# Kernel optimization log

Hardware: AMD Instinct MI355X
Metric: run time of the kernel (lower is better)

The kernel has to match this reference:

```python
import jax, jax.numpy as jnp
import numpy as np

N_NODES = 50000
N_EDGES = 800000
HIDDEN = 128
N_LAYERS = 3
MAX_Z = 1000
N_GRAPHS = 512
LN_EPS = 1e-5


def setup_inputs() -> dict:
    key = jax.random.key(0)
    ks = jax.random.split(key, 16)
    s = 0.05
    inp = {
        "z": jax.random.randint(ks[0], (N_NODES,), 0, MAX_Z),
        "edge_index": jax.random.randint(ks[1], (2, N_EDGES), 0, N_NODES),
        "batch": jnp.sort(jax.random.randint(ks[2], (N_NODES,), 0, N_GRAPHS)),
        "z_table": jax.random.normal(ks[3], (MAX_Z, HIDDEN), jnp.float32) * s,
        "W1": jax.random.normal(ks[4], (N_LAYERS, HIDDEN, HIDDEN), jnp.float32) * s,
        "b1": jnp.zeros((N_LAYERS, HIDDEN), jnp.float32),
        "W2": jax.random.normal(ks[5], (N_LAYERS, HIDDEN, HIDDEN), jnp.float32) * s,
        "b2": jnp.zeros((N_LAYERS, HIDDEN), jnp.float32),
        "ln_g": jnp.ones((N_LAYERS, HIDDEN), jnp.float32),
        "ln_b": jnp.zeros((N_LAYERS, HIDDEN), jnp.float32),
        "lin1_W": jax.random.normal(ks[6], (N_LAYERS * HIDDEN, HIDDEN), jnp.float32) * s,
        "lin1_b": jnp.zeros((HIDDEN,), jnp.float32),
        "lin2_W": jax.random.normal(ks[7], (HIDDEN, 1), jnp.float32) * s,
        "lin2_b": jnp.zeros((1,), jnp.float32),
    }
    return inp


def _layernorm(h, g, b):
    mu = jnp.mean(h, axis=-1, keepdims=True)
    var = jnp.mean((h - mu) ** 2, axis=-1, keepdims=True)
    return g * (h - mu) * jax.lax.rsqrt(var + LN_EPS) + b


def _gin_conv(x, src, dst, W1, b1, W2, b2, g, b):
    # sum-aggregate neighbor features, eps = 0 (train_eps=False)
    agg = jax.ops.segment_sum(x[src], dst, num_segments=N_NODES)
    h = x + agg
    h = jax.nn.relu(h @ W1 + b1)
    h = jax.nn.relu(h @ W2 + b2)
    return _layernorm(h, g, b)


def reference(z, edge_index, batch, z_table, W1, b1, W2, b2, ln_g, ln_b,
              lin1_W, lin1_b, lin2_W, lin2_b):
    src, dst = edge_index[0], edge_index[1]
    x = z_table[z]  # [N, H] z embedding (z is 1-D so no sum over dim 1)
    xs = []
    for l in range(N_LAYERS):
        x = _gin_conv(x, src, dst, W1[l], b1[l], W2[l], b2[l], ln_g[l], ln_b[l])
        xs.append(x)
    xcat = jnp.concatenate(xs, axis=1)  # JK concat [N, L*H]
    # global mean pool over graphs
    sums = jax.ops.segment_sum(xcat, batch, num_segments=N_GRAPHS)
    cnts = jax.ops.segment_sum(jnp.ones((N_NODES, 1), xcat.dtype), batch,
                               num_segments=N_GRAPHS)
    pooled = sums / jnp.maximum(cnts, 1.0)
    h = jax.nn.relu(pooled @ lin1_W + lin1_b)
    # dropout is identity in eval mode
    return h @ lin2_W + lin2_b  # [N_GRAPHS, 1]
```

## Files before the change

kernel.cpp:

```cpp
#include <hip/hip_runtime.h>
#include <hip/hip_bf16.h>

#define NN 50000
#define NE 800000
#define HD 128
#define NL 3
#define NG 512
#define LN_EPS 1e-5f
#define NXCD 8
#define NPX 6250

typedef unsigned short u16;
typedef unsigned int u32;
typedef __attribute__((ext_vector_type(8))) short short8;
typedef __attribute__((ext_vector_type(4))) float f32x4;

__device__ __forceinline__ u16 f2bf(float f){
  u32 x = __float_as_uint(f);
  u32 r = (x + 0x7fffu + ((x >> 16) & 1u)) >> 16;
  return (u16)r;
}
__device__ __forceinline__ float blo(u32 u){ return __uint_as_float(u << 16); }
__device__ __forceinline__ float bhi(u32 u){ return __uint_as_float(u & 0xffff0000u); }
__device__ __forceinline__ u32 pk2(float a, float b){ return (u32)f2bf(a) | ((u32)f2bf(b) << 16); }

__device__ __forceinline__ int lower_bound_dev(const int* a, int n, int v){
  int lo = 0, hi = n;
  while (lo < hi){ int m = (lo + hi) >> 1; if (a[m] < v) lo = m + 1; else hi = m; }
  return lo;
}

__global__ __launch_bounds__(256) void k_prep_w(const float* __restrict__ W1,
    const float* __restrict__ W2, u16* __restrict__ Wt){
  int t = blockIdx.x * 256 + threadIdx.x;
  if (t >= 6 * 128 * 128) return;
  int w = t >> 14, r = t & 16383, n = r >> 7, k = r & 127;
  int l = w >> 1;
  const float* Ws = (w & 1) ? (W2 + l * 16384) : (W1 + l * 16384);
  Wt[t] = f2bf(Ws[k * 128 + n]);
}

__global__ __launch_bounds__(256) void k_embed(const int* __restrict__ z,
    const float* __restrict__ tab, u16* __restrict__ xb){
  int gt = blockIdx.x * 256 + threadIdx.x;
  int node = gt >> 5, q = gt & 31;
  float4 v = *reinterpret_cast<const float4*>(tab + (size_t)z[node] * 128 + q * 4);
  uint2 p = { pk2(v.x, v.y), pk2(v.z, v.w) };
  *reinterpret_cast<uint2*>(xb + (size_t)node * 128 + q * 4) = p;
}

__global__ __launch_bounds__(256) void k_count(const int* __restrict__ dst,
    int* __restrict__ deg){
  int xcd = blockIdx.x & 7;
  int grp = blockIdx.x >> 3;
  int nlo = xcd * NPX, nhi = nlo + NPX;
  for (int e = grp * 256 + threadIdx.x; e < NE; e += 128 * 256){
    int d = dst[e];
    if (d >= nlo && d < nhi) atomicAdd(&deg[d], 1);
  }
}

__global__ __launch_bounds__(256) void k_scan1(const int* __restrict__ deg,
    int* __restrict__ part, int* __restrict__ bsum){
  int i = blockIdx.x * 256 + threadIdx.x;
  int v = (i < NN) ? deg[i] : 0;
  int lane = threadIdx.x & 63, wave = threadIdx.x >> 6;
  int s = v;
  for (int off = 1; off < 64; off <<= 1){ int n = __shfl_up(s, off); if (lane >= off) s += n; }
  __shared__ int wsums[4];
  if (lane == 63) wsums[wave] = s;
  __syncthreads();
  int add = 0;
  for (int w = 0; w < wave; ++w) add += wsums[w];
  int incl = s + add;
  if (i < NN) part[i] = incl - v;
  if (threadIdx.x == 255) bsum[blockIdx.x] = incl;
}

__global__ __launch_bounds__(256) void k_scan2(int* __restrict__ bsum, int nb){
  int tid = threadIdx.x;
  int v = (tid < nb) ? bsum[tid] : 0;
  int lane = tid & 63, wave = tid >> 6;
  int s = v;
  for (int off = 1; off < 64; off <<= 1){ int n = __shfl_up(s, off); if (lane >= off) s += n; }
  __shared__ int wsums[4];
  if (lane == 63) wsums[wave] = s;
  __syncthreads();
  int add = 0;
  for (int w = 0; w < wave; ++w) add += wsums[w];
  int incl = s + add;
  if (tid < nb) bsum[tid] = incl - v;
}

__global__ __launch_bounds__(256) void k_scan3(const int* __restrict__ part,
    const int* __restrict__ bsum, int* __restrict__ rowptr, int* __restrict__ cursor){
  int i = blockIdx.x * 256 + threadIdx.x;
  if (i < NN){ int r = part[i] + bsum[blockIdx.x]; rowptr[i] = r; cursor[i] = r; }
  if (i == 0) rowptr[NN] = NE;
}

__global__ __launch_bounds__(256) void k_fill(const int* __restrict__ src,
    const int* __restrict__ dst, int* __restrict__ cursor, u16* __restrict__ col){
  int xcd = blockIdx.x & 7;
  int grp = blockIdx.x >> 3;
  int nlo = xcd * NPX, nhi = nlo + NPX;
  for (int e = grp * 256 + threadIdx.x; e < NE; e += 128 * 256){
    int d = dst[e];
    if (d >= nlo && d < nhi){
      int p = atomicAdd(&cursor[d], 1);
      col[p] = (u16)src[e];
    }
  }
}

__global__ __launch_bounds__(256) void k_gather(const int* __restrict__ rowptr,
    const u16* __restrict__ col, const u16* __restrict__ xb, u16* __restrict__ hb){
  int wave = threadIdx.x >> 6, lane = threadIdx.x & 63;
  int node = blockIdx.x * 4 + wave;
  int q = lane >> 4, l4 = lane & 15;
  float a[8] = {0.f,0.f,0.f,0.f,0.f,0.f,0.f,0.f};
  float b[8] = {0.f,0.f,0.f,0.f,0.f,0.f,0.f,0.f};
  if (q == 0){
    uint4 s = *reinterpret_cast<const uint4*>(xb + (size_t)node * 128 + l4 * 8);
    a[0] = blo(s.x); a[1] = bhi(s.x); a[2] = blo(s.y); a[3] = bhi(s.y);
    a[4] = blo(s.z); a[5] = bhi(s.z); a[6] = blo(s.w); a[7] = bhi(s.w);
  }
  int lo = rowptr[node], hi = rowptr[node + 1];
  int e = lo + q;
  for (; e + 4 < hi; e += 8){
    int c0 = col[e], c1 = col[e + 4];
    uint4 v0 = *reinterpret_cast<const uint4*>(xb + (size_t)c0 * 128 + l4 * 8);
    uint4 v1 = *reinterpret_cast<const uint4*>(xb + (size_t)c1 * 128 + l4 * 8);
    a[0] += blo(v0.x); a[1] += bhi(v0.x); a[2] += blo(v0.y); a[3] += bhi(v0.y);
    a[4] += blo(v0.z); a[5] += bhi(v0.z); a[6] += blo(v0.w); a[7] += bhi(v0.w);
    b[0] += blo(v1.x); b[1] += bhi(v1.x); b[2] += blo(v1.y); b[3] += bhi(v1.y);
    b[4] += blo(v1.z); b[5] += bhi(v1.z); b[6] += blo(v1.w); b[7] += bhi(v1.w);
  }
  if (e < hi){
    int c0 = col[e];
    uint4 v0 = *reinterpret_cast<const uint4*>(xb + (size_t)c0 * 128 + l4 * 8);
    a[0] += blo(v0.x); a[1] += bhi(v0.x); a[2] += blo(v0.y); a[3] += bhi(v0.y);
    a[4] += blo(v0.z); a[5] += bhi(v0.z); a[6] += blo(v0.w); a[7] += bhi(v0.w);
  }
  #pragma unroll
  for (int j = 0; j < 8; ++j){
    a[j] += b[j];
    a[j] += __shfl_xor(a[j], 16);
    a[j] += __shfl_xor(a[j], 32);
  }
  if (q == 0){
    uint4 p = { pk2(a[0], a[1]), pk2(a[2], a[3]), pk2(a[4], a[5]), pk2(a[6], a[7]) };
    *reinterpret_cast<uint4*>(hb + (size_t)node * 128 + l4 * 8) = p;
  }
}

__global__ __launch_bounds__(256) void k_layer(const u16* __restrict__ A,
    const u16* __restrict__ Wt1, const u16* __restrict__ Wt2,
    const float* __restrict__ bias1, const float* __restrict__ bias2,
    const float* __restrict__ lng, const float* __restrict__ lnb,
    u16* __restrict__ Cout){
  __shared__ u16 As[128 * 128];
  __shared__ u16 Ws[128 * 128];
  int tid = threadIdx.x;
  int rb = blockIdx.x * 128;

  #pragma unroll
  for (int i = 0; i < 8; ++i){
    int u = tid + i * 256;
    int n = u >> 4, k8 = u & 15;
    uint4 w = *reinterpret_cast<const uint4*>(Wt1 + n * 128 + k8 * 8);
    *reinterpret_cast<uint4*>(&Ws[n * 128 + (k8 ^ (n & 15)) * 8]) = w;
  }
  #pragma unroll
  for (int i = 0; i < 8; ++i){
    int u = tid + i * 256;
    int row = u >> 4, k8 = u & 15;
    int grow = rb + row;
    uint4 v = {0u, 0u, 0u, 0u};
    if (grow < NN) v = *reinterpret_cast<const uint4*>(A + (size_t)grow * 128 + k8 * 8);
    *reinterpret_cast<uint4*>(&As[row * 128 + (k8 ^ (row & 15)) * 8]) = v;
  }
  __syncthreads();

  uint4 w2r[8];
  #pragma unroll
  for (int i = 0; i < 8; ++i){
    int u = tid + i * 256;
    int n = u >> 4, k8 = u & 15;
    w2r[i] = *reinterpret_cast<const uint4*>(Wt2 + n * 128 + k8 * 8);
  }

  int wave = tid >> 6, lane = tid & 63;
  int lrow = lane & 15, kgrp = lane >> 4;
  f32x4 acc[2][8];
  #pragma unroll
  for (int rt = 0; rt < 2; ++rt)
    #pragma unroll
    for (int nt = 0; nt < 8; ++nt) acc[rt][nt] = (f32x4){0.f, 0.f, 0.f, 0.f};

  #pragma unroll
  for (int ks = 0; ks < 4; ++ks){
    int ch = ks * 4 + kgrp;
    short8 a0 = *reinterpret_cast<const short8*>(&As[(wave * 32 + lrow) * 128 + (ch ^ lrow) * 8]);
    short8 a1 = *reinterpret_cast<const short8*>(&As[(wave * 32 + 16 + lrow) * 128 + (ch ^ lrow) * 8]);
    #pragma unroll
    for (int nt = 0; nt < 8; ++nt){
      short8 b = *reinterpret_cast<const short8*>(&Ws[(nt * 16 + lrow) * 128 + (ch ^ lrow) * 8]);
      acc[0][nt] = __builtin_amdgcn_mfma_f32_16x16x32_bf16(a0, b, acc[0][nt], 0, 0, 0);
      acc[1][nt] = __builtin_amdgcn_mfma_f32_16x16x32_bf16(a1, b, acc[1][nt], 0, 0, 0);
    }
  }

  #pragma unroll
  for (int nt = 0; nt < 8; ++nt){
    float bv = __ldg(bias1 + nt * 16 + lrow);
    #pragma unroll
    for (int rt = 0; rt < 2; ++rt)
      #pragma unroll
      for (int j = 0; j < 4; ++j)
        acc[rt][nt][j] = fmaxf(acc[rt][nt][j] + bv, 0.f);
  }

  __syncthreads();

  #pragma unroll
  for (int i = 0; i < 8; ++i){
    int u = tid + i * 256;
    int n = u >> 4, k8 = u & 15;
    *reinterpret_cast<uint4*>(&Ws[n * 128 + (k8 ^ (n & 15)) * 8]) = w2r[i];
  }
  #pragma unroll
  for (int rt = 0; rt < 2; ++rt)
    #pragma unroll
    for (int j = 0; j < 4; ++j){
      int row = wave * 32 + rt * 16 + kgrp * 4 + j;
      #pragma unroll
      for (int nt = 0; nt < 8; ++nt){
        int col = nt * 16 + lrow;
        int ch = (col >> 3) ^ (row & 15);
        As[row * 128 + ch * 8 + (col & 7)] = f2bf(acc[rt][nt][j]);
      }
    }
  __syncthreads();

  #pragma unroll
  for (int rt = 0; rt < 2; ++rt)
    #pragma unroll
    for (int nt = 0; nt < 8; ++nt) acc[rt][nt] = (f32x4){0.f, 0.f, 0.f, 0.f};

  #pragma unroll
  for (int ks = 0; ks < 4; ++ks){
    int ch = ks * 4 + kgrp;
    short8 a0 = *reinterpret_cast<const short8*>(&As[(wave * 32 + lrow) * 128 + (ch ^ lrow) * 8]);
    short8 a1 = *reinterpret_cast<const short8*>(&As[(wave * 32 + 16 + lrow) * 128 + (ch ^ lrow) * 8]);
    #pragma unroll
    for (int nt = 0; nt < 8; ++nt){
      short8 b = *reinterpret_cast<const short8*>(&Ws[(nt * 16 + lrow) * 128 + (ch ^ lrow) * 8]);
      acc[0][nt] = __builtin_amdgcn_mfma_f32_16x16x32_bf16(a0, b, acc[0][nt], 0, 0, 0);
      acc[1][nt] = __builtin_amdgcn_mfma_f32_16x16x32_bf16(a1, b, acc[1][nt], 0, 0, 0);
    }
  }

  float gv[8], lbv[8];
  #pragma unroll
  for (int nt = 0; nt < 8; ++nt){
    int gcol = nt * 16 + lrow;
    float bv = __ldg(bias2 + gcol);
    gv[nt] = __ldg(lng + gcol); lbv[nt] = __ldg(lnb + gcol);
    #pragma unroll
    for (int rt = 0; rt < 2; ++rt)
      #pragma unroll
      for (int j = 0; j < 4; ++j)
        acc[rt][nt][j] = fmaxf(acc[rt][nt][j] + bv, 0.f);
  }
  #pragma unroll
  for (int rt = 0; rt < 2; ++rt)
    #pragma unroll
    for (int j = 0; j < 4; ++j){
      float s = 0.f, sq = 0.f;
      #pragma unroll
      for (int nt = 0; nt < 8; ++nt){ float v = acc[rt][nt][j]; s += v; sq += v * v; }
      #pragma unroll
      for (int off = 1; off < 16; off <<= 1){
        s += __shfl_xor(s, off); sq += __shfl_xor(sq, off);
      }
      float mu = s * (1.f / 128.f);
      float var = sq * (1.f / 128.f) - mu * mu;
      float rstd = rsqrtf(var + LN_EPS);
      #pragma unroll
      for (int nt = 0; nt < 8; ++nt)
        acc[rt][nt][j] = gv[nt] * (acc[rt][nt][j] - mu) * rstd + lbv[nt];
    }

  #pragma unroll
  for (int rt = 0; rt < 2; ++rt){
    int rbase = rb + wave * 32 + rt * 16 + kgrp * 4;
    #pragma unroll
    for (int nt = 0; nt < 8; ++nt){
      int gcol = nt * 16 + lrow;
      #pragma unroll
      for (int j = 0; j < 4; ++j){
        int grow = rbase + j;
        if (grow < NN) Cout[(size_t)grow * 128 + gcol] = f2bf(acc[rt][nt][j]);
      }
    }
  }
}

__global__ __launch_bounds__(256) void k_pool(const u16* __restrict__ xb,
    const int* __restrict__ batch, float* __restrict__ pooled, int lslice){
  int g = blockIdx.x;
  int w = threadIdx.x >> 6, lane = threadIdx.x & 63;
  __shared__ float red[4][128];
  int lo = lower_bound_dev(batch, NN, g);
  int hi = lower_bound_dev(batch, NN, g + 1);
  float s0 = 0.f, s1 = 0.f;
  for (int i = lo + w; i < hi; i += 4){
    u32 u = *reinterpret_cast<const u32*>(xb + (size_t)i * 128 + lane * 2);
    s0 += blo(u); s1 += bhi(u);
  }
  red[w][lane * 2] = s0; red[w][lane * 2 + 1] = s1;
  __syncthreads();
  int f = threadIdx.x;
  if (f < 128)
    pooled[(size_t)g * 384 + lslice * 128 + f] = red[0][f] + red[1][f] + red[2][f] + red[3][f];
}

__global__ __launch_bounds__(128) void k_final(const float* __restrict__ pooled,
    const int* __restrict__ batch, const float* __restrict__ W1,
    const float* __restrict__ b1, const float* __restrict__ W2,
    const float* __restrict__ b2, float* __restrict__ out){
  int g = blockIdx.x, f = threadIdx.x;
  int lo = lower_bound_dev(batch, NN, g);
  int hi = lower_bound_dev(batch, NN, g + 1);
  float scale = 1.f / fmaxf((float)(hi - lo), 1.f);
  __shared__ float p[384];
  for (int k = f; k < 384; k += 128) p[k] = pooled[(size_t)g * 384 + k] * scale;
  __syncthreads();
  float acc = __ldg(b1 + f);
  for (int k = 0; k < 384; ++k) acc += p[k] * __ldg(W1 + k * 128 + f);
  float hval = fmaxf(acc, 0.f);
  float v = hval * __ldg(W2 + f);
  for (int off = 32; off; off >>= 1) v += __shfl_xor(v, off);
  __shared__ float red[2];
  int lane = f & 63, wave = f >> 6;
  if (lane == 0) red[wave] = v;
  __syncthreads();
  if (f == 0) out[g] = red[0] + red[1] + __ldg(b2);
}

extern "C" void kernel_launch(void* const* d_in, const int* in_sizes, int n_in,
                              void* d_out, int out_size, void* d_ws, size_t ws_size,
                              hipStream_t stream){
  const int*   z     = (const int*)d_in[0];
  const int*   ei    = (const int*)d_in[1];
  const int*   batch = (const int*)d_in[2];
  const float* ztab  = (const float*)d_in[3];
  const float* W1    = (const float*)d_in[4];
  const float* b1    = (const float*)d_in[5];
  const float* W2    = (const float*)d_in[6];
  const float* b2    = (const float*)d_in[7];
  const float* lng   = (const float*)d_in[8];
  const float* lnb   = (const float*)d_in[9];
  const float* l1W   = (const float*)d_in[10];
  const float* l1b   = (const float*)d_in[11];
  const float* l2W   = (const float*)d_in[12];
  const float* l2b   = (const float*)d_in[13];
  float* out = (float*)d_out;

  char* wsb = (char*)d_ws;
  size_t off = 0;
  auto alloc = [&](size_t bytes){ void* p = wsb + off; off += (bytes + 255) & ~(size_t)255; return p; };
  u16*   xbf    = (u16*)alloc((size_t)NN * 128 * 2);
  u16*   hbf    = (u16*)alloc((size_t)NN * 128 * 2);
  float* pooled = (float*)alloc((size_t)NG * 384 * 4);
  u16*   Wt     = (u16*)alloc((size_t)6 * 128 * 128 * 2);
  int*   deg    = (int*)alloc((size_t)NN * 4);
  int*   part   = (int*)alloc((size_t)NN * 4);
  int*   bsum   = (int*)alloc((size_t)256 * 4);
  int*   rowptr = (int*)alloc((size_t)(NN + 1) * 4);
  int*   cursor = (int*)alloc((size_t)NN * 4);
  u16*   col    = (u16*)alloc((size_t)NE * 2);

  const int* srcv = ei;
  const int* dstv = ei + NE;

  hipMemsetAsync(deg, 0, (size_t)NN * 4, stream);
  k_prep_w<<<(6 * 128 * 128 + 255) / 256, 256, 0, stream>>>(W1, W2, Wt);
  k_embed<<<NN * 32 / 256, 256, 0, stream>>>(z, ztab, xbf);
  k_count<<<1024, 256, 0, stream>>>(dstv, deg);
  int nb = (NN + 255) / 256;
  k_scan1<<<nb, 256, 0, stream>>>(deg, part, bsum);
  k_scan2<<<1, 256, 0, stream>>>(bsum, nb);
  k_scan3<<<nb, 256, 0, stream>>>(part, bsum, rowptr, cursor);
  k_fill<<<1024, 256, 0, stream>>>(srcv, dstv, cursor, col);

  int gb = (NN + 127) / 128;
  for (int l = 0; l < NL; ++l){
    k_gather<<<NN / 4, 256, 0, stream>>>(rowptr, col, xbf, hbf);
    k_layer<<<gb, 256, 0, stream>>>(hbf,
        Wt + (size_t)(l * 2 + 0) * 16384, Wt + (size_t)(l * 2 + 1) * 16384,
        b1 + l * 128, b2 + l * 128, lng + l * 128, lnb + l * 128, xbf);
    k_pool<<<NG, 256, 0, stream>>>(xbf, batch, pooled, l);
  }
  k_final<<<NG, 128, 0, stream>>>(pooled, batch, l1W, l1b, l2W, l2b, out);
}
```

Before: 410.8 us.

## Fuse mean-pool into layer kernel via atomics and unroll gather loop deeper

Result: no change. 413.2 us (+0.6%).

```diff
diff --git a/kernel.cpp b/kernel.cpp
--- a/kernel.cpp
+++ b/kernel.cpp
@@ -127,16 +127,22 @@
   }
   int lo = rowptr[node], hi = rowptr[node + 1];
   int e = lo + q;
-  for (; e + 4 < hi; e += 8){
-    int c0 = col[e], c1 = col[e + 4];
+  for (; e + 12 < hi; e += 16){
+    int c0 = col[e], c1 = col[e + 4], c2 = col[e + 8], c3 = col[e + 12];
     uint4 v0 = *reinterpret_cast<const uint4*>(xb + (size_t)c0 * 128 + l4 * 8);
     uint4 v1 = *reinterpret_cast<const uint4*>(xb + (size_t)c1 * 128 + l4 * 8);
+    uint4 v2 = *reinterpret_cast<const uint4*>(xb + (size_t)c2 * 128 + l4 * 8);
+    uint4 v3 = *reinterpret_cast<const uint4*>(xb + (size_t)c3 * 128 + l4 * 8);
     a[0] += blo(v0.x); a[1] += bhi(v0.x); a[2] += blo(v0.y); a[3] += bhi(v0.y);
     a[4] += blo(v0.z); a[5] += bhi(v0.z); a[6] += blo(v0.w); a[7] += bhi(v0.w);
     b[0] += blo(v1.x); b[1] += bhi(v1.x); b[2] += blo(v1.y); b[3] += bhi(v1.y);
     b[4] += blo(v1.z); b[5] += bhi(v1.z); b[6] += blo(v1.w); b[7] += bhi(v1.w);
-  }
-  if (e < hi){
+    a[0] += blo(v2.x); a[1] += bhi(v2.x); a[2] += blo(v2.y); a[3] += bhi(v2.y);
+    a[4] += blo(v2.z); a[5] += bhi(v2.z); a[6] += blo(v2.w); a[7] += bhi(v2.w);
+    b[0] += blo(v3.x); b[1] += bhi(v3.x); b[2] += blo(v3.y); b[3] += bhi(v3.y);
+    b[4] += blo(v3.z); b[5] += bhi(v3.z); b[6] += blo(v3.w); b[7] += bhi(v3.w);
+  }
+  for (; e < hi; e += 4){
     int c0 = col[e];
     uint4 v0 = *reinterpret_cast<const uint4*>(xb + (size_t)c0 * 128 + l4 * 8);
     a[0] += blo(v0.x); a[1] += bhi(v0.x); a[2] += blo(v0.y); a[3] += bhi(v0.y);
@@ -158,9 +164,11 @@
     const u16* __restrict__ Wt1, const u16* __restrict__ Wt2,
     const float* __restrict__ bias1, const float* __restrict__ bias2,
     const float* __restrict__ lng, const float* __restrict__ lnb,
-    u16* __restrict__ Cout){
+    u16* __restrict__ Cout, const int* __restrict__ batch,
+    float* __restrict__ pooled, int lsl){
   __shared__ u16 As[128 * 128];
   __shared__ u16 Ws[128 * 128];
+  __shared__ int sb[128];
   int tid = threadIdx.x;
   int rb = blockIdx.x * 128;
 
@@ -180,6 +188,10 @@
     if (grow < NN) v = *reinterpret_cast<const uint4*>(A + (size_t)grow * 128 + k8 * 8);
     *reinterpret_cast<uint4*>(&As[row * 128 + (k8 ^ (row & 15)) * 8]) = v;
   }
+  if (tid < 128){
+    int grow = rb + tid;
+    sb[tid] = (grow < NN) ? batch[grow] : -1;
+  }
   __syncthreads();
 
   uint4 w2r[8];
@@ -305,25 +317,29 @@
       }
     }
   }
-}
-
-__global__ __launch_bounds__(256) void k_pool(const u16* __restrict__ xb,
-    const int* __restrict__ batch, float* __restrict__ pooled, int lslice){
-  int g = blockIdx.x;
-  int w = threadIdx.x >> 6, lane = threadIdx.x & 63;
-  __shared__ float red[4][128];
-  int lo = lower_bound_dev(batch, NN, g);
-  int hi = lower_bound_dev(batch, NN, g + 1);
-  float s0 = 0.f, s1 = 0.f;
-  for (int i = lo + w; i < hi; i += 4){
-    u32 u = *reinterpret_cast<const u32*>(xb + (size_t)i * 128 + lane * 2);
-    s0 += blo(u); s1 += bhi(u);
-  }
-  red[w][lane * 2] = s0; red[w][lane * 2 + 1] = s1;
-  __syncthreads();
-  int f = threadIdx.x;
-  if (f < 128)
-    pooled[(size_t)g * 384 + lslice * 128 + f] = red[0][f] + red[1][f] + red[2][f] + red[3][f];
+
+  __syncthreads();
+  #pragma unroll
+  for (int rt = 0; rt < 2; ++rt)
+    #pragma unroll
+    for (int j = 0; j < 4; ++j){
+      int row = wave * 32 + rt * 16 + kgrp * 4 + j;
+      #pragma unroll
+      for (int nt = 0; nt < 8; ++nt)
+        As[row * 128 + nt * 16 + lrow] = f2bf(acc[rt][nt][j]);
+    }
+  __syncthreads();
+  int f = tid & 127, half = tid >> 7;
+  int cur = -1; float sum = 0.f;
+  for (int r = half * 64; r < half * 64 + 64; ++r){
+    int g = sb[r];
+    if (g != cur){
+      if (cur >= 0) atomicAdd(&pooled[(size_t)cur * 384 + lsl * 128 + f], sum);
+      cur = g; sum = 0.f;
+    }
+    if (g >= 0) sum += blo((u32)As[r * 128 + f]);
+  }
+  if (cur >= 0) atomicAdd(&pooled[(size_t)cur * 384 + lsl * 128 + f], sum);
 }
 
 __global__ __launch_bounds__(128) void k_final(const float* __restrict__ pooled,
@@ -373,9 +389,9 @@
   auto alloc = [&](size_t bytes){ void* p = wsb + off; off += (bytes + 255) & ~(size_t)255; return p; };
   u16*   xbf    = (u16*)alloc((size_t)NN * 128 * 2);
   u16*   hbf    = (u16*)alloc((size_t)NN * 128 * 2);
-  float* pooled = (float*)alloc((size_t)NG * 384 * 4);
   u16*   Wt     = (u16*)alloc((size_t)6 * 128 * 128 * 2);
   int*   deg    = (int*)alloc((size_t)NN * 4);
+  float* pooled = (float*)alloc((size_t)NG * 384 * 4);
   int*   part   = (int*)alloc((size_t)NN * 4);
   int*   bsum   = (int*)alloc((size_t)256 * 4);
   int*   rowptr = (int*)alloc((size_t)(NN + 1) * 4);
@@ -385,7 +401,8 @@
   const int* srcv = ei;
   const int* dstv = ei + NE;
 
-  hipMemsetAsync(deg, 0, (size_t)NN * 4, stream);
+  size_t zero_bytes = ((size_t)NN * 4 + 255 & ~(size_t)255) + (size_t)NG * 384 * 4;
+  hipMemsetAsync(deg, 0, zero_bytes, stream);
   k_prep_w<<<(6 * 128 * 128 + 255) / 256, 256, 0, stream>>>(W1, W2, Wt);
   k_embed<<<NN * 32 / 256, 256, 0, stream>>>(z, ztab, xbf);
   k_count<<<1024, 256, 0, stream>>>(dstv, deg);
@@ -400,8 +417,8 @@
     k_gather<<<NN / 4, 256, 0, stream>>>(rowptr, col, xbf, hbf);
     k_layer<<<gb, 256, 0, stream>>>(hbf,
         Wt + (size_t)(l * 2 + 0) * 16384, Wt + (size_t)(l * 2 + 1) * 16384,
-        b1 + l * 128, b2 + l * 128, lng + l * 128, lnb + l * 128, xbf);
-    k_pool<<<NG, 256, 0, stream>>>(xbf, batch, pooled, l);
+        b1 + l * 128, b2 + l * 128, lng + l * 128, lnb + l * 128, xbf,
+        batch, pooled, l);
   }
   k_final<<<NG, 128, 0, stream>>>(pooled, batch, l1W, l1b, l2W, l2b, out);
 }
```
